# Optimization experiments

Hardware: AMD Instinct MI355X
Metric: run time of the kernel (lower is better)

The kernel has to match this reference:

```python
import jax, jax.numpy as jnp
import numpy as np

N_NODE = 40000
EMB = 100
LAYERS = 2
B = 512
L = 50
N = 50
E = 800000


def _l2norm(x, axis=-1, eps=1e-12):
    n = jnp.sqrt(jnp.sum(x * x, axis=axis, keepdims=True))
    return x / jnp.maximum(n, eps)


def _item_conv(rows, cols, vals, emb, b):
    # sparse A @ X repeated LAYERS times, stack, l2-normalize rows, weighted sum
    finals = [emb]
    x = emb
    for _ in range(LAYERS):
        x = jax.ops.segment_sum(vals[:, None] * x[cols], rows, num_segments=emb.shape[0])
        finals.append(x)
    f = _l2norm(jnp.stack(finals, 0))                      # [LAYERS+1, n, d]
    return jnp.sum(b[:, None, None] * f, axis=0)


def _session_conv(adj_dense, emb, a):
    finals = [emb]
    x = emb
    for _ in range(LAYERS):
        x = adj_dense @ x
        finals.append(x)
    f = _l2norm(jnp.stack(finals, 0))
    return jnp.sum(a[:, None, None] * f, axis=0)


def _gat(h, adj, a0, a1, a2, a3):
    # e_k[b,i,j] = leakyrelu(sum_d h[b,i,d]*h[b,j,d]*a_k[d]); never materialize [B,N,N,D]
    def score(a):
        return jax.nn.leaky_relu(jnp.einsum('bid,bjd->bij', h * a[:, 0], h), 0.2)
    e0, e1, e2, e3 = score(a0), score(a1), score(a2), score(a3)
    neg = jnp.float32(-9e15)
    alpha = jnp.where(adj == 1, e0, neg)
    alpha = jnp.where(adj == 2, e1, alpha)
    alpha = jnp.where(adj == 3, e2, alpha)
    alpha = jnp.where(adj == 4, e3, alpha)
    alpha = jax.nn.softmax(alpha, axis=-1)
    return jnp.einsum('bij,bjd->bid', alpha, h)


def _get_seq(emb_table, rev, h, alias, mix=0.8):
    seq_h = emb_table[rev]                                  # [B,L,D]
    bidx = jnp.arange(rev.shape[0])[:, None]
    seq_h_ = h[bidx, alias]                                 # [B,L,D]
    return (1.0 - mix) * seq_h + mix * seq_h_               # eval: dropout = identity


def _soft_attention(seq_h, mask_f, session_len, pos_emb, w1_W, w1_b, glu1_W, glu1_b, glu2_W, w2):
    hs = jnp.sum(seq_h, axis=1) / session_len               # [B,D]
    pos = jnp.broadcast_to(pos_emb[:seq_h.shape[1]][None], seq_h.shape)
    nh = jnp.tanh(jnp.concatenate([pos, seq_h], -1) @ w1_W.T + w1_b)
    nh = jax.nn.sigmoid(nh @ glu1_W.T + glu1_b + (hs @ glu2_W.T)[:, None, :])
    beta = (nh @ w2) * mask_f[..., None]                    # [B,L,1]
    return jnp.sum(beta * seq_h, axis=1)                    # [B,D]


def setup_inputs() -> dict:
    key = jax.random.key(0)
    ks = jax.random.split(key, 30)
    stdv = 1.0 / np.sqrt(EMB)
    u = lambda k, s: jax.random.uniform(k, s, jnp.float32, -stdv, stdv)
    return {
        'tar': jax.random.randint(ks[0], (B,), 0, N_NODE),
        'reversed_sess_item': jax.random.randint(ks[1], (B, L), 0, N_NODE + 1),
        'mask': jnp.ones((B, L), jnp.int32),
        'session_len': jnp.ones((B, 1), jnp.float32),
        'session_adj': jax.random.uniform(ks[2], (B, B), jnp.float32),
        'is_train': 0,
        'items': jax.random.randint(ks[3], (B, N), 0, N_NODE + 1),
        'adj': jax.random.randint(ks[4], (B, N, N), 0, 5),
        'alias_session': jax.random.randint(ks[5], (B, L), 0, N),
        'gnn_rows': jax.random.randint(ks[6], (E,), 0, N_NODE),
        'gnn_cols': jax.random.randint(ks[7], (E,), 0, N_NODE),
        'gnn_vals': jax.random.uniform(ks[8], (E,), jnp.float32),
        'nodes_emb': u(ks[9], (N_NODE, EMB)),
        'b_item': jnp.ones((LAYERS + 1,), jnp.float32),
        'a_sess': jnp.ones((LAYERS + 1,), jnp.float32),
        'a0': u(ks[10], (EMB, 1)), 'a1': u(ks[11], (EMB, 1)),
        'a2': u(ks[12], (EMB, 1)), 'a3': u(ks[13], (EMB, 1)),
        'w1_W': u(ks[14], (EMB, 2 * EMB)), 'w1_b': u(ks[15], (EMB,)),
        'w2': u(ks[16], (EMB, 1)),
        'glu1_W': u(ks[17], (EMB, EMB)), 'glu1_b': u(ks[18], (EMB,)),
        'glu2_W': u(ks[19], (EMB, EMB)),
        'pos_emb': u(ks[20], (150, EMB)),
    }


def reference(tar, reversed_sess_item, mask, session_len, session_adj, is_train,
              items, adj, alias_session, gnn_rows, gnn_cols, gnn_vals,
              nodes_emb, b_item, a_sess, a0, a1, a2, a3,
              w1_W, w1_b, w2, glu1_W, glu1_b, glu2_W, pos_emb):
    mask_f = mask.astype(jnp.float32)
    zeros = jnp.zeros((1, EMB), jnp.float32)
    emb_gnn = _item_conv(gnn_rows, gnn_cols, gnn_vals, nodes_emb, b_item)
    # eval mode: both dropouts are identity
    e1t = jnp.concatenate([zeros, emb_gnn], 0)
    e2t = jnp.concatenate([zeros, emb_gnn], 0)
    embeddings = e1t + e2t

    h1 = _gat(e1t[items], adj, a0, a1, a2, a3)
    h1 = _get_seq(e1t, reversed_sess_item, h1, alias_session, 0.8)
    h2 = _gat(e2t[items], adj, a0, a1, a2, a3)
    h2 = _get_seq(e2t, reversed_sess_item, h2, alias_session, 0.8)

    sel1 = _soft_attention(h1, mask_f, session_len, pos_emb, w1_W, w1_b, glu1_W, glu1_b, glu2_W, w2)
    sel1 = _session_conv(session_adj, sel1, a_sess)
    sel2 = _soft_attention(h2, mask_f, session_len, pos_emb, w1_W, w1_b, glu1_W, glu1_b, glu2_W, w2)
    sel2 = _session_conv(session_adj, sel2, a_sess)

    con_loss = jnp.float32(0.0)  # is_train == 0 (inference path)

    seq_h = sel1 + sel2
    scores = seq_h @ embeddings[1:].T                       # [B, N_NODE]
    logp = jax.nn.log_softmax(scores + 1e-8, axis=-1)
    loss = -jnp.mean(logp[jnp.arange(scores.shape[0]), tar])
    return (con_loss, loss, scores)
```

## Files before the change

### kernel.cpp

```cpp
#include <hip/hip_runtime.h>
#include <hip/hip_bf16.h>
#include <math.h>

#define N_NODE 40000
#define EMB 100
#define BB 512
#define LL 50
#define NI 50
#define EDG 800000
#define SCAN_BLOCKS 157

typedef short s16x8 __attribute__((ext_vector_type(8)));
typedef float f32x4 __attribute__((ext_vector_type(4)));

__global__ void khist(const int* __restrict__ rows, int* __restrict__ counts) {
  int e = blockIdx.x * 256 + threadIdx.x;
  atomicAdd(&counts[rows[e]], 1);
}

__global__ __launch_bounds__(256) void kscan1(const int* __restrict__ counts,
                                              int* __restrict__ scanout,
                                              int* __restrict__ blocksums, int n) {
  __shared__ int wsum[4];
  int tid = threadIdx.x;
  int i = blockIdx.x * 256 + tid;
  int v = (i < n) ? counts[i] : 0;
  int x = v;
  #pragma unroll
  for (int off = 1; off < 64; off <<= 1) {
    int t = __shfl_up(x, off, 64);
    if ((tid & 63) >= off) x += t;
  }
  int w = tid >> 6, lane = tid & 63;
  if (lane == 63) wsum[w] = x;
  __syncthreads();
  int woff = 0;
  #pragma unroll
  for (int k = 0; k < 4; ++k) woff += (k < w) ? wsum[k] : 0;
  int incl = x + woff;
  if (i < n) scanout[i] = incl - v;
  if (tid == 255) blocksums[blockIdx.x] = incl;
}

__global__ __launch_bounds__(256) void kscan2(int* __restrict__ blocksums, int nb) {
  __shared__ int wsum[4];
  int tid = threadIdx.x;
  int v = (tid < nb) ? blocksums[tid] : 0;
  int x = v;
  #pragma unroll
  for (int off = 1; off < 64; off <<= 1) {
    int t = __shfl_up(x, off, 64);
    if ((tid & 63) >= off) x += t;
  }
  int w = tid >> 6, lane = tid & 63;
  if (lane == 63) wsum[w] = x;
  __syncthreads();
  int woff = 0;
  #pragma unroll
  for (int k = 0; k < 4; ++k) woff += (k < w) ? wsum[k] : 0;
  if (tid < nb) blocksums[tid] = x + woff - v;
}

__global__ __launch_bounds__(256) void kscan3(const int* __restrict__ scanout,
                                              const int* __restrict__ blocksums,
                                              int* __restrict__ starts,
                                              int* __restrict__ cursor, int n) {
  int i = blockIdx.x * 256 + threadIdx.x;
  if (i < n) {
    int s = scanout[i] + blocksums[blockIdx.x];
    starts[i] = s;
    cursor[i] = s;
  }
}

__global__ __launch_bounds__(256) void kfill(const int* __restrict__ rows,
                                             const int* __restrict__ cols,
                                             const float* __restrict__ vals,
                                             int* __restrict__ cursor,
                                             int2* __restrict__ colval) {
  int e0 = (blockIdx.x * 256 + threadIdx.x) * 4;
  #pragma unroll
  for (int k = 0; k < 4; ++k) {
    int e = e0 + k;
    if (e < EDG) {
      int r = rows[e];
      int p = atomicAdd(&cursor[r], 1);
      int2 cv; cv.x = cols[e]; cv.y = __float_as_int(vals[e]);
      colval[p] = cv;
    }
  }
}

__global__ __launch_bounds__(256) void kspmm(const int* __restrict__ starts,
                                             const int* __restrict__ counts,
                                             const int2* __restrict__ colval,
                                             const float* __restrict__ x,
                                             float* __restrict__ out) {
  int row = blockIdx.x * 4 + (threadIdx.x >> 6);
  int lane = threadIdx.x & 63;
  int s = starts[row], cnt = counts[row];
  bool act = lane < 50;
  int d2 = (act ? lane : 49) * 2;
  float ax = 0.f, ay = 0.f;
  for (int base = 0; base < cnt; base += 64) {
    int nb = cnt - base; if (nb > 64) nb = 64;
    int cl = 0; float vl = 0.f;
    if (lane < nb) {
      int2 cv = colval[s + base + lane];
      cl = cv.x; vl = __int_as_float(cv.y);
    }
    int t = 0;
    for (; t + 8 <= nb; t += 8) {
      int c0 = __shfl(cl, t),     c1 = __shfl(cl, t + 1);
      int c2 = __shfl(cl, t + 2), c3 = __shfl(cl, t + 3);
      int c4 = __shfl(cl, t + 4), c5 = __shfl(cl, t + 5);
      int c6 = __shfl(cl, t + 6), c7 = __shfl(cl, t + 7);
      float v0 = __shfl(vl, t),     v1 = __shfl(vl, t + 1);
      float v2 = __shfl(vl, t + 2), v3 = __shfl(vl, t + 3);
      float v4 = __shfl(vl, t + 4), v5 = __shfl(vl, t + 5);
      float v6 = __shfl(vl, t + 6), v7 = __shfl(vl, t + 7);
      float2 g0 = *(const float2*)(x + (size_t)c0 * EMB + d2);
      float2 g1 = *(const float2*)(x + (size_t)c1 * EMB + d2);
      float2 g2 = *(const float2*)(x + (size_t)c2 * EMB + d2);
      float2 g3 = *(const float2*)(x + (size_t)c3 * EMB + d2);
      float2 g4 = *(const float2*)(x + (size_t)c4 * EMB + d2);
      float2 g5 = *(const float2*)(x + (size_t)c5 * EMB + d2);
      float2 g6 = *(const float2*)(x + (size_t)c6 * EMB + d2);
      float2 g7 = *(const float2*)(x + (size_t)c7 * EMB + d2);
      ax += v0 * g0.x; ay += v0 * g0.y;
      ax += v1 * g1.x; ay += v1 * g1.y;
      ax += v2 * g2.x; ay += v2 * g2.y;
      ax += v3 * g3.x; ay += v3 * g3.y;
      ax += v4 * g4.x; ay += v4 * g4.y;
      ax += v5 * g5.x; ay += v5 * g5.y;
      ax += v6 * g6.x; ay += v6 * g6.y;
      ax += v7 * g7.x; ay += v7 * g7.y;
    }
    for (; t + 4 <= nb; t += 4) {
      int c0 = __shfl(cl, t),     c1 = __shfl(cl, t + 1);
      int c2 = __shfl(cl, t + 2), c3 = __shfl(cl, t + 3);
      float v0 = __shfl(vl, t),     v1 = __shfl(vl, t + 1);
      float v2 = __shfl(vl, t + 2), v3 = __shfl(vl, t + 3);
      float2 g0 = *(const float2*)(x + (size_t)c0 * EMB + d2);
      float2 g1 = *(const float2*)(x + (size_t)c1 * EMB + d2);
      float2 g2 = *(const float2*)(x + (size_t)c2 * EMB + d2);
      float2 g3 = *(const float2*)(x + (size_t)c3 * EMB + d2);
      ax += v0 * g0.x; ay += v0 * g0.y;
      ax += v1 * g1.x; ay += v1 * g1.y;
      ax += v2 * g2.x; ay += v2 * g2.y;
      ax += v3 * g3.x; ay += v3 * g3.y;
    }
    for (; t < nb; ++t) {
      int c = __shfl(cl, t);
      float v = __shfl(vl, t);
      float2 g = *(const float2*)(x + (size_t)c * EMB + d2);
      ax += v * g.x; ay += v * g.y;
    }
  }
  if (act) {
    float2 o; o.x = ax; o.y = ay;
    *(float2*)(out + (size_t)row * EMB + d2) = o;
  }
}

__global__ void kcomb(const float* __restrict__ x0, const float* __restrict__ x1,
                      const float* __restrict__ x2, const float* __restrict__ bI,
                      float* __restrict__ emb) {
  int n = blockIdx.x * 4 + (threadIdx.x >> 6);
  int lane = threadIdx.x & 63;
  int d0 = lane, d1 = lane + 64;
  bool h1 = d1 < EMB;
  size_t base = (size_t)n * EMB;
  float v00 = x0[base + d0], v01 = h1 ? x0[base + d1] : 0.f;
  float v10 = x1[base + d0], v11 = h1 ? x1[base + d1] : 0.f;
  float v20 = x2[base + d0], v21 = h1 ? x2[base + d1] : 0.f;
  float q0 = v00 * v00 + v01 * v01;
  float q1 = v10 * v10 + v11 * v11;
  float q2 = v20 * v20 + v21 * v21;
  #pragma unroll
  for (int off = 32; off; off >>= 1) {
    q0 += __shfl_xor(q0, off);
    q1 += __shfl_xor(q1, off);
    q2 += __shfl_xor(q2, off);
  }
  float r0 = 1.f / fmaxf(sqrtf(q0), 1e-12f);
  float r1 = 1.f / fmaxf(sqrtf(q1), 1e-12f);
  float r2 = 1.f / fmaxf(sqrtf(q2), 1e-12f);
  float b0 = bI[0], b1 = bI[1], b2 = bI[2];
  emb[base + d0] = b0 * v00 * r0 + b1 * v10 * r1 + b2 * v20 * r2;
  if (h1) emb[base + d1] = b0 * v01 * r0 + b1 * v11 * r1 + b2 * v21 * r2;
}

__global__ __launch_bounds__(256) void kgat(
    const float* __restrict__ emb, const int* __restrict__ items,
    const int* __restrict__ adj,
    const float* __restrict__ a0p, const float* __restrict__ a1p,
    const float* __restrict__ a2p, const float* __restrict__ a3p,
    float* __restrict__ hgat) {
  __shared__ __align__(16) float hl[64 * 108];
  __shared__ __align__(16) float as[4 * 100];
  __shared__ float alpha_lds[64 * 51];
  __shared__ float wred[4][2][64];
  int b = blockIdx.x;
  int tid = threadIdx.x;
  for (int idx = tid; idx < 400; idx += 256) {
    int k = idx / 100, d = idx % 100;
    const float* ap = (k == 0) ? a0p : (k == 1) ? a1p : (k == 2) ? a2p : a3p;
    as[idx] = ap[d];
  }
  for (int idx = tid; idx < 64 * 50; idx += 256) {
    int i = idx / 50, d2 = (idx % 50) * 2;
    float2 v; v.x = 0.f; v.y = 0.f;
    if (i < NI) {
      int node = items[b * NI + i];
      if (node != 0) v = *(const float2*)(emb + (size_t)(node - 1) * EMB + d2);
    }
    *(float2*)&hl[i * 108 + d2] = v;
  }
  __syncthreads();
  int w = tid >> 6, lane = tid & 63;
  int j0 = w * 13;
  int nj = 50 - j0; if (nj > 13) nj = 13;

  float4 hreg[25];
  #pragma unroll
  for (int q = 0; q < 25; ++q) hreg[q] = *(const float4*)&hl[lane * 108 + q * 4];

  int al_lane = (lane < NI) ? lane : NI - 1;
  const int* adjrow = adj + (size_t)b * (NI * NI) + al_lane * NI + j0;
  int adjv[13];
  #pragma unroll
  for (int t = 0; t < 13; ++t) adjv[t] = (t < nj) ? adjrow[t] : 0;

  float e[13];
  #pragma unroll
  for (int jj = 0; jj < 13; ++jj) {
    float acc = 0.f;
    if (jj < nj) {
      int j = j0 + jj;
      int k = adjv[jj] - 1; k = (k < 0) ? 0 : (k > 3) ? 3 : k;
      const float* aw = &as[k * 100];
      #pragma unroll
      for (int q = 0; q < 25; ++q) {
        float4 hj = *(const float4*)&hl[j * 108 + q * 4];
        float4 a4 = *(const float4*)(aw + q * 4);
        float4 hm = hreg[q];
        acc += hm.x * hj.x * a4.x + hm.y * hj.y * a4.y
             + hm.z * hj.z * a4.z + hm.w * hj.w * a4.w;
      }
      acc = (acc >= 0.f) ? acc : 0.2f * acc;
      acc = (adjv[jj] == 0) ? -9e15f : acc;
    } else {
      acc = -INFINITY;
    }
    e[jj] = acc;
  }

  float mloc = -INFINITY;
  #pragma unroll
  for (int jj = 0; jj < 13; ++jj) if (jj < nj) mloc = fmaxf(mloc, e[jj]);
  wred[w][0][lane] = mloc;
  __syncthreads();
  float m = fmaxf(fmaxf(wred[0][0][lane], wred[1][0][lane]),
                  fmaxf(wred[2][0][lane], wred[3][0][lane]));
  float sloc = 0.f;
  #pragma unroll
  for (int jj = 0; jj < 13; ++jj) if (jj < nj) {
    e[jj] = expf(e[jj] - m);
    sloc += e[jj];
  }
  wred[w][1][lane] = sloc;
  __syncthreads();
  float s = (wred[0][1][lane] + wred[1][1][lane]) +
            (wred[2][1][lane] + wred[3][1][lane]);
  float inv = 1.f / s;
  #pragma unroll
  for (int jj = 0; jj < 13; ++jj) if (jj < nj)
    alpha_lds[lane * 51 + j0 + jj] = e[jj] * inv;
  __syncthreads();

  int nq = (w == 0) ? 7 : 6;
  float4 outq[7];
  #pragma unroll
  for (int t = 0; t < 7; ++t) outq[t] = make_float4(0.f, 0.f, 0.f, 0.f);
  for (int j = 0; j < NI; ++j) {
    float aj = alpha_lds[lane * 51 + j];
    #pragma unroll
    for (int t = 0; t < 7; ++t) {
      if (t < nq) {
        int q = w + 4 * t;
        float4 hv = *(const float4*)&hl[j * 108 + q * 4];
        outq[t].x += aj * hv.x; outq[t].y += aj * hv.y;
        outq[t].z += aj * hv.z; outq[t].w += aj * hv.w;
      }
    }
  }
  if (lane < NI) {
    #pragma unroll
    for (int t = 0; t < 7; ++t) {
      if (t < nq) {
        int q = w + 4 * t;
        *(float4*)&hgat[((size_t)b * NI + lane) * EMB + q * 4] = outq[t];
      }
    }
  }
}

__global__ void kseq(const float* __restrict__ emb, const int* __restrict__ rev,
                     const int* __restrict__ alias, const float* __restrict__ hgat,
                     float* __restrict__ hseq) {
  int idx = blockIdx.x * 256 + threadIdx.x;
  int b = idx / 5000, r = idx % 5000, l = r / 100, d = r % 100;
  int node = rev[b * LL + l];
  float sh = (node == 0) ? 0.f : emb[(size_t)(node - 1) * EMB + d];
  int a = alias[b * LL + l];
  float shh = hgat[((size_t)b * NI + a) * EMB + d];
  hseq[idx] = 0.2f * sh + 0.8f * shh;
}

__global__ void kprep_t(const float* __restrict__ w1W, const float* __restrict__ g1W,
                        const float* __restrict__ g2W, float* __restrict__ w1t2,
                        float* __restrict__ g1t, float* __restrict__ g2t) {
  int idx = blockIdx.x * 256 + threadIdx.x;
  if (idx >= 10000) return;
  int c = idx / 100, o = idx % 100;
  w1t2[c * 100 + o] = w1W[o * 200 + 100 + c];
  g1t[c * 100 + o] = g1W[o * 100 + c];
  g2t[c * 100 + o] = g2W[o * 100 + c];
}

__global__ void kprep_pos(const float* __restrict__ posE, const float* __restrict__ w1W,
                          const float* __restrict__ w1b, float* __restrict__ posW) {
  int idx = blockIdx.x * 256 + threadIdx.x;
  if (idx >= 5000) return;
  int l = idx / 100, o = idx % 100;
  float acc = w1b[o];
  for (int c = 0; c < 100; ++c) acc += posE[l * 100 + c] * w1W[o * 200 + c];
  posW[idx] = acc;
}

__global__ __launch_bounds__(256) void ksoft(
    const float* __restrict__ hseqG, const float* __restrict__ slenp,
    const int* __restrict__ maskp,
    const float* __restrict__ posW, const float* __restrict__ w1t2,
    const float* __restrict__ glu1t, const float* __restrict__ glu1b,
    const float* __restrict__ glu2t, const float* __restrict__ w2,
    float* __restrict__ sel) {
  __shared__ float hq[LL * 101];
  __shared__ float nh[LL * 100];
  __shared__ float red[25 * 52];
  __shared__ float hs_s[100];
  __shared__ float g_s[100];
  __shared__ float beta_s[LL];
  int b = blockIdx.x, tid = threadIdx.x;
  for (int idx = tid; idx < LL * 100; idx += 256) {
    int l = idx / 100, d = idx % 100;
    hq[l * 101 + d] = hseqG[((size_t)b * LL + l) * 100 + d];
  }
  __syncthreads();
  if (tid < 100) {
    float s = 0.f;
    for (int l = 0; l < LL; ++l) s += hq[l * 101 + tid];
    hs_s[tid] = s / slenp[b];
  }
  __syncthreads();
  if (tid < 100) {
    float acc = 0.f;
    for (int c = 0; c < 100; ++c) acc += hs_s[c] * glu2t[c * 100 + tid];
    g_s[tid] = acc;
  }
  int lg = tid / 25, og = tid % 25;
  if (tid < 250) {
    float acc[5][4];
    #pragma unroll
    for (int j = 0; j < 5; ++j) {
      float4 p = *(const float4*)&posW[(lg * 5 + j) * 100 + og * 4];
      acc[j][0] = p.x; acc[j][1] = p.y; acc[j][2] = p.z; acc[j][3] = p.w;
    }
    for (int c = 0; c < 100; ++c) {
      float4 wv = *(const float4*)&w1t2[c * 100 + og * 4];
      float hv[5];
      #pragma unroll
      for (int j = 0; j < 5; ++j) hv[j] = hq[(lg * 5 + j) * 101 + c];
      #pragma unroll
      for (int j = 0; j < 5; ++j) {
        acc[j][0] += hv[j] * wv.x;
        acc[j][1] += hv[j] * wv.y;
        acc[j][2] += hv[j] * wv.z;
        acc[j][3] += hv[j] * wv.w;
      }
    }
    #pragma unroll
    for (int j = 0; j < 5; ++j) {
      float4 t;
      t.x = tanhf(acc[j][0]); t.y = tanhf(acc[j][1]);
      t.z = tanhf(acc[j][2]); t.w = tanhf(acc[j][3]);
      *(float4*)&nh[(lg * 5 + j) * 100 + og * 4] = t;
    }
  }
  __syncthreads();
  if (tid < 250) {
    float4 gb = *(const float4*)&glu1b[og * 4];
    float4 gg = *(const float4*)&g_s[og * 4];
    float base0 = gg.x + gb.x, base1 = gg.y + gb.y, base2 = gg.z + gb.z, base3 = gg.w + gb.w;
    float acc[5][4];
    #pragma unroll
    for (int j = 0; j < 5; ++j) {
      acc[j][0] = base0; acc[j][1] = base1; acc[j][2] = base2; acc[j][3] = base3;
    }
    for (int c = 0; c < 100; ++c) {
      float4 wv = *(const float4*)&glu1t[c * 100 + og * 4];
      float hv[5];
      #pragma unroll
      for (int j = 0; j < 5; ++j) hv[j] = nh[(lg * 5 + j) * 100 + c];
      #pragma unroll
      for (int j = 0; j < 5; ++j) {
        acc[j][0] += hv[j] * wv.x;
        acc[j][1] += hv[j] * wv.y;
        acc[j][2] += hv[j] * wv.z;
        acc[j][3] += hv[j] * wv.w;
      }
    }
    float4 w2v = *(const float4*)&w2[og * 4];
    #pragma unroll
    for (int j = 0; j < 5; ++j) {
      float s0 = w2v.x / (1.f + expf(-acc[j][0]));
      float s1 = w2v.y / (1.f + expf(-acc[j][1]));
      float s2 = w2v.z / (1.f + expf(-acc[j][2]));
      float s3 = w2v.w / (1.f + expf(-acc[j][3]));
      red[og * 52 + lg * 5 + j] = (s0 + s1) + (s2 + s3);
    }
  }
  __syncthreads();
  if (tid < LL) {
    float s = 0.f;
    for (int og2 = 0; og2 < 25; ++og2) s += red[og2 * 52 + tid];
    beta_s[tid] = s * (float)maskp[b * LL + tid];
  }
  __syncthreads();
  if (tid < 100) {
    float acc = 0.f;
    for (int l = 0; l < LL; ++l) acc += beta_s[l] * hq[l * 101 + tid];
    sel[(size_t)b * 100 + tid] = acc;
  }
}

__global__ void ksess(const float* __restrict__ adjS, const float* __restrict__ x,
                      float* __restrict__ out) {
  int b = blockIdx.x, d = threadIdx.x;
  if (d >= 100) return;
  const float* ar = adjS + (size_t)b * BB;
  float a0 = 0.f, a1 = 0.f, a2 = 0.f, a3 = 0.f;
  for (int j = 0; j < BB; j += 4) {
    a0 += ar[j]     * x[(j)     * 100 + d];
    a1 += ar[j + 1] * x[(j + 1) * 100 + d];
    a2 += ar[j + 2] * x[(j + 2) * 100 + d];
    a3 += ar[j + 3] * x[(j + 3) * 100 + d];
  }
  out[(size_t)b * 100 + d] = (a0 + a1) + (a2 + a3);
}

__global__ void ksesscomb(const float* __restrict__ x0, const float* __restrict__ x1,
                          const float* __restrict__ x2, const float* __restrict__ aS,
                          float* __restrict__ out) {
  int b = blockIdx.x * 4 + (threadIdx.x >> 6);
  int lane = threadIdx.x & 63;
  int d0 = lane, d1 = lane + 64;
  bool h1 = d1 < EMB;
  size_t base = (size_t)b * EMB;
  float v00 = x0[base + d0], v01 = h1 ? x0[base + d1] : 0.f;
  float v10 = x1[base + d0], v11 = h1 ? x1[base + d1] : 0.f;
  float v20 = x2[base + d0], v21 = h1 ? x2[base + d1] : 0.f;
  float q0 = v00 * v00 + v01 * v01;
  float q1 = v10 * v10 + v11 * v11;
  float q2 = v20 * v20 + v21 * v21;
  #pragma unroll
  for (int off = 32; off; off >>= 1) {
    q0 += __shfl_xor(q0, off);
    q1 += __shfl_xor(q1, off);
    q2 += __shfl_xor(q2, off);
  }
  float r0 = 1.f / fmaxf(sqrtf(q0), 1e-12f);
  float r1 = 1.f / fmaxf(sqrtf(q1), 1e-12f);
  float r2 = 1.f / fmaxf(sqrtf(q2), 1e-12f);
  float b0 = aS[0], b1 = aS[1], b2 = aS[2];
  out[base + d0] = 2.f * (b0 * v00 * r0 + b1 * v10 * r1 + b2 * v20 * r2);
  if (h1) out[base + d1] = 2.f * (b0 * v01 * r0 + b1 * v11 * r1 + b2 * v21 * r2);
}

__global__ void kprepB(const float* __restrict__ emb, unsigned short* __restrict__ bHi,
                       unsigned short* __restrict__ bLo) {
  int idx = blockIdx.x * 256 + threadIdx.x;
  int n = idx >> 7, k = idx & 127;
  float v = (k < EMB) ? 2.f * emb[(size_t)n * EMB + k] : 0.f;
  __hip_bfloat16 h = __float2bfloat16(v);
  float rem = v - __bfloat162float(h);
  __hip_bfloat16 l = __float2bfloat16(rem);
  bHi[idx] = *reinterpret_cast<unsigned short*>(&h);
  bLo[idx] = *reinterpret_cast<unsigned short*>(&l);
}

__global__ void kprepA(const float* __restrict__ seqh, unsigned short* __restrict__ aHi,
                       unsigned short* __restrict__ aLo) {
  int idx = blockIdx.x * 256 + threadIdx.x;
  int n = idx >> 7, k = idx & 127;
  float v = (k < EMB) ? seqh[(size_t)n * EMB + k] : 0.f;
  __hip_bfloat16 h = __float2bfloat16(v);
  float rem = v - __bfloat162float(h);
  __hip_bfloat16 l = __float2bfloat16(rem);
  aHi[idx] = *reinterpret_cast<unsigned short*>(&h);
  aLo[idx] = *reinterpret_cast<unsigned short*>(&l);
}

__global__ __launch_bounds__(256) void kscoresM(
    const unsigned short* __restrict__ aHi, const unsigned short* __restrict__ aLo,
    const unsigned short* __restrict__ bHi, const unsigned short* __restrict__ bLo,
    float* __restrict__ outS) {
  __shared__ __align__(16) unsigned short Bh[32 * 136];
  __shared__ __align__(16) unsigned short Bl[32 * 136];
  int tid = threadIdx.x;
  int n0 = blockIdx.x * 32;
  int w = tid >> 6, lane = tid & 63;
  int ln = lane & 15, quad = lane >> 4;

  #pragma unroll
  for (int it = 0; it < 2; ++it) {
    int seg = tid + it * 256;
    int r = seg >> 4, q = seg & 15;
    *(s16x8*)&Bh[r * 136 + q * 8] = *(const s16x8*)&bHi[(size_t)(n0 + r) * 128 + q * 8];
    *(s16x8*)&Bl[r * 136 + q * 8] = *(const s16x8*)&bLo[(size_t)(n0 + r) * 128 + q * 8];
  }
  __syncthreads();

  for (int b0 = 0; b0 < BB; b0 += 64) {
    const unsigned short* aRowH = aHi + (size_t)(b0 + w * 16 + ln) * 128 + quad * 8;
    const unsigned short* aRowL = aLo + (size_t)(b0 + w * 16 + ln) * 128 + quad * 8;
    s16x8 ah[4], al[4];
    #pragma unroll
    for (int s = 0; s < 4; ++s) {
      ah[s] = *(const s16x8*)(aRowH + s * 32);
      al[s] = *(const s16x8*)(aRowL + s * 32);
    }
    f32x4 acc[2];
    #pragma unroll
    for (int t = 0; t < 2; ++t) acc[t] = (f32x4){0.f, 0.f, 0.f, 0.f};
    #pragma unroll
    for (int s = 0; s < 4; ++s) {
      #pragma unroll
      for (int t = 0; t < 2; ++t) {
        s16x8 bh = *(const s16x8*)&Bh[(t * 16 + ln) * 136 + s * 32 + quad * 8];
        s16x8 bl = *(const s16x8*)&Bl[(t * 16 + ln) * 136 + s * 32 + quad * 8];
        acc[t] = __builtin_amdgcn_mfma_f32_16x16x32_bf16(ah[s], bh, acc[t], 0, 0, 0);
        acc[t] = __builtin_amdgcn_mfma_f32_16x16x32_bf16(al[s], bh, acc[t], 0, 0, 0);
        acc[t] = __builtin_amdgcn_mfma_f32_16x16x32_bf16(ah[s], bl, acc[t], 0, 0, 0);
      }
    }
    int brow = b0 + w * 16 + quad * 4;
    #pragma unroll
    for (int t = 0; t < 2; ++t) {
      int ncol = n0 + t * 16 + ln;
      #pragma unroll
      for (int r = 0; r < 4; ++r) {
        outS[(size_t)(brow + r) * N_NODE + ncol] = acc[t][r];
      }
    }
  }
}

__global__ __launch_bounds__(256) void klse(const float* __restrict__ outS,
                                            const int* __restrict__ tar,
                                            float* __restrict__ part) {
  __shared__ float ms[256], ss[256];
  int b = blockIdx.x, tid = threadIdx.x;
  const float2* sp = (const float2*)(outS + (size_t)b * N_NODE);
  float m = -INFINITY, s = 0.f;
  for (int i = tid; i < N_NODE / 2; i += 256) {
    float2 v = sp[i];
    float mx = fmaxf(v.x, v.y);
    float add = expf(v.x - mx) + expf(v.y - mx);
    if (mx > m) { s = s * expf(m - mx) + add; m = mx; }
    else s += add * expf(mx - m);
  }
  ms[tid] = m; ss[tid] = s;
  __syncthreads();
  for (int st = 128; st; st >>= 1) {
    if (tid < st) {
      float m2 = ms[tid + st], s2 = ss[tid + st];
      float M = fmaxf(ms[tid], m2);
      ss[tid] = ss[tid] * expf(ms[tid] - M) + s2 * expf(m2 - M);
      ms[tid] = M;
    }
    __syncthreads();
  }
  if (tid == 0) {
    float tsc = outS[(size_t)b * N_NODE + tar[b]];
    part[b] = tsc - (ms[0] + logf(ss[0]));
  }
}

__global__ void kfinal(const float* __restrict__ part, float* __restrict__ out) {
  __shared__ float red[256];
  int tid = threadIdx.x;
  red[tid] = part[tid] + part[tid + 256];
  __syncthreads();
  for (int st = 128; st; st >>= 1) {
    if (tid < st) red[tid] += red[tid + st];
    __syncthreads();
  }
  if (tid == 0) {
    out[0] = 0.f;
    out[1] = -red[0] / (float)BB;
  }
}

extern "C" void kernel_launch(void* const* d_in, const int* in_sizes, int n_in,
                              void* d_out, int out_size, void* d_ws, size_t ws_size,
                              hipStream_t stream) {
  const int* tar    = (const int*)d_in[0];
  const int* rev    = (const int*)d_in[1];
  const int* maskp  = (const int*)d_in[2];
  const float* slen = (const float*)d_in[3];
  const float* sadj = (const float*)d_in[4];
  const int* items  = (const int*)d_in[6];
  const int* adjp   = (const int*)d_in[7];
  const int* alias  = (const int*)d_in[8];
  const int* grows  = (const int*)d_in[9];
  const int* gcols  = (const int*)d_in[10];
  const float* gvals = (const float*)d_in[11];
  const float* nemb = (const float*)d_in[12];
  const float* bI   = (const float*)d_in[13];
  const float* aS   = (const float*)d_in[14];
  const float* a0p  = (const float*)d_in[15];
  const float* a1p  = (const float*)d_in[16];
  const float* a2p  = (const float*)d_in[17];
  const float* a3p  = (const float*)d_in[18];
  const float* w1W  = (const float*)d_in[19];
  const float* w1b  = (const float*)d_in[20];
  const float* w2p  = (const float*)d_in[21];
  const float* g1W  = (const float*)d_in[22];
  const float* g1b  = (const float*)d_in[23];
  const float* g2W  = (const float*)d_in[24];
  const float* posE = (const float*)d_in[25];

  float* W = (float*)d_ws;
  size_t o = 0;
  float* emb_gnn = W + o; o += (size_t)N_NODE * EMB;
  float* x1      = W + o; o += (size_t)N_NODE * EMB;
  float* x2      = W + o; o += (size_t)N_NODE * EMB;
  float* sel     = W + o; o += (size_t)BB * EMB;
  float* y1      = W + o; o += (size_t)BB * EMB;
  float* y2      = W + o; o += (size_t)BB * EMB;
  float* seqh    = W + o; o += (size_t)BB * EMB;
  float* posW    = W + o; o += 5120;
  float* w1t2    = W + o; o += 10000;
  float* glu1t   = W + o; o += 10000;
  float* glu2t   = W + o; o += 10000;
  int2* colval   = (int2*)(W + o); o += (size_t)2 * EDG;
  float* part    = W + o; o += 512;
  int* counts = (int*)(W + o); o += N_NODE;
  int* starts = (int*)(W + o); o += N_NODE;
  int* cursor = (int*)(W + o); o += N_NODE;
  int* scantmp = (int*)(W + o); o += N_NODE;
  int* blocksums = (int*)(W + o); o += 256;
  unsigned short* aHi = (unsigned short*)(W + o); o += 32768;
  unsigned short* aLo = (unsigned short*)(W + o); o += 32768;
  float* hgat = x1;
  float* hseq = x2;
  unsigned short* bHi = (unsigned short*)x1;
  unsigned short* bLo = (unsigned short*)x2;

  float* outF = (float*)d_out;
  float* outScores = outF + 2;

  hipMemsetAsync(counts, 0, N_NODE * sizeof(int), stream);
  khist<<<EDG / 256, 256, 0, stream>>>(grows, counts);
  kscan1<<<SCAN_BLOCKS, 256, 0, stream>>>(counts, scantmp, blocksums, N_NODE);
  kscan2<<<1, 256, 0, stream>>>(blocksums, SCAN_BLOCKS);
  kscan3<<<SCAN_BLOCKS, 256, 0, stream>>>(scantmp, blocksums, starts, cursor, N_NODE);
  kfill<<<(EDG + 1023) / 1024, 256, 0, stream>>>(grows, gcols, gvals, cursor, colval);
  kspmm<<<N_NODE / 4, 256, 0, stream>>>(starts, counts, colval, nemb, x1);
  kspmm<<<N_NODE / 4, 256, 0, stream>>>(starts, counts, colval, x1, x2);
  kcomb<<<N_NODE / 4, 256, 0, stream>>>(nemb, x1, x2, bI, emb_gnn);
  kgat<<<BB, 256, 0, stream>>>(emb_gnn, items, adjp, a0p, a1p, a2p, a3p, hgat);
  kseq<<<(BB * LL * EMB) / 256, 256, 0, stream>>>(emb_gnn, rev, alias, hgat, hseq);
  kprep_t<<<40, 256, 0, stream>>>(w1W, g1W, g2W, w1t2, glu1t, glu2t);
  kprep_pos<<<20, 256, 0, stream>>>(posE, w1W, w1b, posW);
  ksoft<<<BB, 256, 0, stream>>>(hseq, slen, maskp, posW, w1t2, glu1t, g1b, glu2t, w2p, sel);
  kprepB<<<(N_NODE * 128) / 256, 256, 0, stream>>>(emb_gnn, bHi, bLo);
  ksess<<<BB, 128, 0, stream>>>(sadj, sel, y1);
  ksess<<<BB, 128, 0, stream>>>(sadj, y1, y2);
  ksesscomb<<<BB / 4, 256, 0, stream>>>(sel, y1, y2, aS, seqh);
  kprepA<<<(BB * 128) / 256, 256, 0, stream>>>(seqh, aHi, aLo);
  kscoresM<<<N_NODE / 32, 256, 0, stream>>>(aHi, aLo, bHi, bLo, outScores);
  klse<<<BB, 256, 0, stream>>>(outScores, tar, part);
  kfinal<<<1, 256, 0, stream>>>(part, outF);
}
```

Before: 560.5 us.

## Retile scores GEMM to 128x64 blocks over a 2D grid

The scores kernel changes from one block per 32 item columns looping over all 512 batch rows to a 2D grid. Each block now covers 128 batch rows by 64 items, holding A fragments in registers and staging a larger B tile in shared memory. The goal is more parallel blocks and fewer redundant A reloads per block, at the cost of more shared memory and registers per block, which may lower occupancy.

```diff
diff --git a/kernel.cpp b/kernel.cpp
--- a/kernel.cpp
+++ b/kernel.cpp
@@ -516,15 +516,29 @@
     const unsigned short* __restrict__ aHi, const unsigned short* __restrict__ aLo,
     const unsigned short* __restrict__ bHi, const unsigned short* __restrict__ bLo,
     float* __restrict__ outS) {
-  __shared__ __align__(16) unsigned short Bh[32 * 136];
-  __shared__ __align__(16) unsigned short Bl[32 * 136];
+  __shared__ __align__(16) unsigned short Bh[64 * 136];
+  __shared__ __align__(16) unsigned short Bl[64 * 136];
   int tid = threadIdx.x;
-  int n0 = blockIdx.x * 32;
+  int n0 = blockIdx.y * 64;
+  int bbase = blockIdx.x * 128;
   int w = tid >> 6, lane = tid & 63;
   int ln = lane & 15, quad = lane >> 4;
 
-  #pragma unroll
-  for (int it = 0; it < 2; ++it) {
+  const unsigned short* aRowH0 = aHi + (size_t)(bbase + w * 16 + ln) * 128 + quad * 8;
+  const unsigned short* aRowL0 = aLo + (size_t)(bbase + w * 16 + ln) * 128 + quad * 8;
+  const unsigned short* aRowH1 = aRowH0 + 64 * 128;
+  const unsigned short* aRowL1 = aRowL0 + 64 * 128;
+  s16x8 ah0[4], al0[4], ah1[4], al1[4];
+  #pragma unroll
+  for (int s = 0; s < 4; ++s) {
+    ah0[s] = *(const s16x8*)(aRowH0 + s * 32);
+    al0[s] = *(const s16x8*)(aRowL0 + s * 32);
+    ah1[s] = *(const s16x8*)(aRowH1 + s * 32);
+    al1[s] = *(const s16x8*)(aRowL1 + s * 32);
+  }
+
+  #pragma unroll
+  for (int it = 0; it < 4; ++it) {
     int seg = tid + it * 256;
     int r = seg >> 4, q = seg & 15;
     *(s16x8*)&Bh[r * 136 + q * 8] = *(const s16x8*)&bHi[(size_t)(n0 + r) * 128 + q * 8];
@@ -532,32 +546,49 @@
   }
   __syncthreads();
 
-  for (int b0 = 0; b0 < BB; b0 += 64) {
-    const unsigned short* aRowH = aHi + (size_t)(b0 + w * 16 + ln) * 128 + quad * 8;
-    const unsigned short* aRowL = aLo + (size_t)(b0 + w * 16 + ln) * 128 + quad * 8;
-    s16x8 ah[4], al[4];
-    #pragma unroll
-    for (int s = 0; s < 4; ++s) {
-      ah[s] = *(const s16x8*)(aRowH + s * 32);
-      al[s] = *(const s16x8*)(aRowL + s * 32);
-    }
-    f32x4 acc[2];
-    #pragma unroll
-    for (int t = 0; t < 2; ++t) acc[t] = (f32x4){0.f, 0.f, 0.f, 0.f};
-    #pragma unroll
-    for (int s = 0; s < 4; ++s) {
+  f32x4 acc[4];
+  #pragma unroll
+  for (int t = 0; t < 4; ++t) acc[t] = (f32x4){0.f, 0.f, 0.f, 0.f};
+  #pragma unroll
+  for (int s = 0; s < 4; ++s) {
+    #pragma unroll
+    for (int t = 0; t < 4; ++t) {
+      s16x8 bh = *(const s16x8*)&Bh[(t * 16 + ln) * 136 + s * 32 + quad * 8];
+      s16x8 bl = *(const s16x8*)&Bl[(t * 16 + ln) * 136 + s * 32 + quad * 8];
+      acc[t] = __builtin_amdgcn_mfma_f32_16x16x32_bf16(ah0[s], bh, acc[t], 0, 0, 0);
+      acc[t] = __builtin_amdgcn_mfma_f32_16x16x32_bf16(al0[s], bh, acc[t], 0, 0, 0);
+      acc[t] = __builtin_amdgcn_mfma_f32_16x16x32_bf16(ah0[s], bl, acc[t], 0, 0, 0);
+    }
+  }
+  {
+    int brow = bbase + w * 16 + quad * 4;
+    #pragma unroll
+    for (int t = 0; t < 4; ++t) {
+      int ncol = n0 + t * 16 + ln;
       #pragma unroll
-      for (int t = 0; t < 2; ++t) {
-        s16x8 bh = *(const s16x8*)&Bh[(t * 16 + ln) * 136 + s * 32 + quad * 8];
-        s16x8 bl = *(const s16x8*)&Bl[(t * 16 + ln) * 136 + s * 32 + quad * 8];
-        acc[t] = __builtin_amdgcn_mfma_f32_16x16x32_bf16(ah[s], bh, acc[t], 0, 0, 0);
-        acc[t] = __builtin_amdgcn_mfma_f32_16x16x32_bf16(al[s], bh, acc[t], 0, 0, 0);
-        acc[t] = __builtin_amdgcn_mfma_f32_16x16x32_bf16(ah[s], bl, acc[t], 0, 0, 0);
+      for (int r = 0; r < 4; ++r) {
+        outS[(size_t)(brow + r) * N_NODE + ncol] = acc[t][r];
       }
     }
-    int brow = b0 + w * 16 + quad * 4;
-    #pragma unroll
-    for (int t = 0; t < 2; ++t) {
+  }
+
+  #pragma unroll
+  for (int t = 0; t < 4; ++t) acc[t] = (f32x4){0.f, 0.f, 0.f, 0.f};
+  #pragma unroll
+  for (int s = 0; s < 4; ++s) {
+    #pragma unroll
+    for (int t = 0; t < 4; ++t) {
+      s16x8 bh = *(const s16x8*)&Bh[(t * 16 + ln) * 136 + s * 32 + quad * 8];
+      s16x8 bl = *(const s16x8*)&Bl[(t * 16 + ln) * 136 + s * 32 + quad * 8];
+      acc[t] = __builtin_amdgcn_mfma_f32_16x16x32_bf16(ah1[s], bh, acc[t], 0, 0, 0);
+      acc[t] = __builtin_amdgcn_mfma_f32_16x16x32_bf16(al1[s], bh, acc[t], 0, 0, 0);
+      acc[t] = __builtin_amdgcn_mfma_f32_16x16x32_bf16(ah1[s], bl, acc[t], 0, 0, 0);
+    }
+  }
+  {
+    int brow = bbase + 64 + w * 16 + quad * 4;
+    #pragma unroll
+    for (int t = 0; t < 4; ++t) {
       int ncol = n0 + t * 16 + ln;
       #pragma unroll
       for (int r = 0; r < 4; ++r) {
@@ -691,7 +722,7 @@
   ksess<<<BB, 128, 0, stream>>>(sadj, y1, y2);
   ksesscomb<<<BB / 4, 256, 0, stream>>>(sel, y1, y2, aS, seqh);
   kprepA<<<(BB * 128) / 256, 256, 0, stream>>>(seqh, aHi, aLo);
-  kscoresM<<<N_NODE / 32, 256, 0, stream>>>(aHi, aLo, bHi, bLo, outScores);
+  kscoresM<<<dim3(4, N_NODE / 64), 256, 0, stream>>>(aHi, aLo, bHi, bLo, outScores);
   klse<<<BB, 256, 0, stream>>>(outScores, tar, part);
   kfinal<<<1, 256, 0, stream>>>(part, outF);
 }
```

Measured after the change: 553.1 us. Within noise of the previous version (-1.3%).
